# Optimization experiments

Hardware: AMD Instinct MI355X
Metric: run time of the kernel (lower is better)

Reference implementation:

```python
import jax, jax.numpy as jnp
import numpy as np

RMS_EPS = 1e-5


def setup_inputs() -> dict:
    key = jax.random.key(0)
    ks = jax.random.split(key, 7)
    B, N, D, H = 8, 1024, 1024, 4
    Dv = D // H
    s = lambda k, shp, fan: jax.random.normal(k, shp, jnp.float32) * (1.0 / np.sqrt(fan))
    return {
        "x": jax.random.normal(ks[0], (B, N, D), jnp.float32),
        "Wq": s(ks[1], (D, D), D),
        "Wk": s(ks[2], (D, D), D),
        "Wv": s(ks[3], (D, D), D),
        "Wbeta": s(ks[4], (D, H), D),
        "Wo": s(ks[5], (D, D), D),
        "g_norm": jnp.ones((Dv,), jnp.float32),
    }


def _l2norm(t):
    return t / jnp.linalg.norm(t, axis=-1, keepdims=True)


def _delta_rule(q, k, v, beta):
    # q,k: [B,H,N,Dk]; v: [B,H,N,Dv]; beta: [B,H,N]
    B, H, N, Dk = q.shape
    Dv = v.shape[-1]
    # time-major for scan: [N,B,H,D]
    qT = jnp.moveaxis(q, 2, 0)
    kT = jnp.moveaxis(k, 2, 0)
    vT = jnp.moveaxis(v, 2, 0)
    bT = jnp.moveaxis(beta, 2, 0)  # [N,B,H]

    def step(S, inp):
        q_t, k_t, v_t, b_t = inp  # [B,H,Dk], [B,H,Dk], [B,H,Dv], [B,H]
        pred = jnp.einsum('bhk,bhkv->bhv', k_t, S)
        err = (v_t - pred) * b_t[..., None]          # delta-rule error, scaled by beta
        S = S + jnp.einsum('bhk,bhv->bhkv', k_t, err)  # rank-1 state update
        o_t = jnp.einsum('bhk,bhkv->bhv', q_t, S)
        return S, o_t

    S0 = jnp.zeros((B, H, Dk, Dv), q.dtype)
    _, oT = jax.lax.scan(step, S0, (qT, kT, vT, bT))
    return jnp.moveaxis(oT, 0, 2)  # [B,H,N,Dv]


def reference(x, Wq, Wk, Wv, Wbeta, Wo, g_norm):
    B, N, D = x.shape
    H = Wbeta.shape[1]
    Dk = Wq.shape[1] // H
    Dv = Wv.shape[1] // H
    split = lambda t, d: t.reshape(B, N, H, d).transpose(0, 2, 1, 3)  # b n (h d) -> b h n d
    q = _l2norm(split(x @ Wq, Dk))
    k = _l2norm(split(x @ Wk, Dk))
    v = split(x @ Wv, Dv)
    beta = jax.nn.sigmoid(x @ Wbeta).transpose(0, 2, 1)  # [B,H,N]
    o = _delta_rule(q, k, v, beta)  # [B,H,N,Dv]
    # per-head RMSNorm over Dv
    o = o * jax.lax.rsqrt(jnp.mean(o * o, axis=-1, keepdims=True) + RMS_EPS) * g_norm
    o = o.transpose(0, 2, 1, 3).reshape(B, N, H * Dv)  # b h n d -> b n (h d)
    return o @ Wo
```

## Files before the change

kernel.cpp:

```cpp
#include <hip/hip_runtime.h>
#include <hip/hip_bf16.h>
#include <math.h>

typedef unsigned short u16;
typedef __attribute__((ext_vector_type(8))) __bf16 bf16x8;
typedef __attribute__((ext_vector_type(4))) float f32x4;

#define MFMA16 __builtin_amdgcn_mfma_f32_16x16x32_bf16

__device__ __forceinline__ float bf2f(unsigned int u) {
    union { unsigned int i; float f; } x;
    x.i = (u & 0xffffu) << 16;
    return x.f;
}
__device__ __forceinline__ u16 f2bf(float f) {
    unsigned int i = __float_as_uint(f);
    unsigned int r = (i + 0x7fffu + ((i >> 16) & 1u)) >> 16;
    return (u16)r;
}

__device__ __forceinline__ void gload_lds16(const void* g, void* l) {
    __builtin_amdgcn_global_load_lds((const __attribute__((address_space(1))) void*)g,
                                     (__attribute__((address_space(3))) void*)l, 16, 0, 0);
}

#define BARS() do { asm volatile("s_waitcnt lgkmcnt(0)" ::: "memory"); \
                    __builtin_amdgcn_s_barrier(); } while (0)
#define SYNCALL() do { asm volatile("s_waitcnt vmcnt(0) lgkmcnt(0)" ::: "memory"); \
                       __builtin_amdgcn_s_barrier(); } while (0)

__global__ void detect_dtype(const unsigned* __restrict__ wq, int* __restrict__ flag)
{
    int lane = threadIdx.x;
    unsigned lo = wq[lane] & 0xffffu;
    unsigned e = (lo >> 7) & 0xffu;
    int m = (e >= 0x6e && e <= 0x7e) ? 1 : 0;
#pragma unroll
    for (int s = 1; s < 64; s <<= 1) m += __shfl_xor(m, s);
    if (lane == 0) flag[0] = (m >= 32) ? 0 : 1;
}

__global__ __launch_bounds__(256) void convert_vec(
    const void* __restrict__ src, u16* __restrict__ dst, int n, const int* __restrict__ flag)
{
    int stride = gridDim.x * 256;
    int i0 = blockIdx.x * 256 + threadIdx.x;
    if (*flag) {
        const float* s = (const float*)src;
        for (int i = i0; i < n; i += stride) dst[i] = f2bf(s[i]);
    } else {
        const u16* s = (const u16*)src;
        for (int i = i0; i < n; i += stride) dst[i] = s[i];
    }
}

__global__ __launch_bounds__(256) void transpose_cvt(
    const void* __restrict__ w0, const void* __restrict__ w1,
    const void* __restrict__ w2, const void* __restrict__ w3,
    u16* __restrict__ o0, u16* __restrict__ o1,
    u16* __restrict__ o2, u16* __restrict__ o3, const int* __restrict__ flag)
{
    const void* in; u16* out;
    switch (blockIdx.z) {
        case 0: in = w0; out = o0; break;
        case 1: in = w1; out = o1; break;
        case 2: in = w2; out = o2; break;
        default: in = w3; out = o3; break;
    }
    int n  = blockIdx.x * 64 + (threadIdx.x & 63);
    int kb = blockIdx.y * 32 + (threadIdx.x >> 6) * 8;
    u16 v[8];
    if (*flag) {
        const float* f = (const float*)in;
#pragma unroll
        for (int j = 0; j < 8; ++j) v[j] = f2bf(f[(size_t)(kb + j) * 1024 + n]);
    } else {
        const u16* s = (const u16*)in;
#pragma unroll
        for (int j = 0; j < 8; ++j) v[j] = s[(size_t)(kb + j) * 1024 + n];
    }
    uint4 pk;
    pk.x = (unsigned)v[0] | ((unsigned)v[1] << 16);
    pk.y = (unsigned)v[2] | ((unsigned)v[3] << 16);
    pk.z = (unsigned)v[4] | ((unsigned)v[5] << 16);
    pk.w = (unsigned)v[6] | ((unsigned)v[7] << 16);
    *(uint4*)(out + (size_t)n * 1024 + kb) = pk;
}

__global__ __launch_bounds__(256) void gemm_bt(
    const u16* __restrict__ A, const u16* __restrict__ BT, void* __restrict__ C,
    int M, int Nn, int K, const int* __restrict__ flag, int fp32_out)
{
    __shared__ alignas(16) u16 As[128 * 32];
    __shared__ alignas(16) u16 Bs[128 * 32];
    const int tid  = threadIdx.x;
    const int lane = tid & 63;
    const int wv   = tid >> 6;
    const int wm   = wv >> 1, wn = wv & 1;
    const int bm   = blockIdx.x * 128, bn = blockIdx.y * 128;
    const int fr   = lane & 15, fk = lane >> 4;

    f32x4 acc[4][4];
#pragma unroll
    for (int i = 0; i < 4; ++i)
#pragma unroll
        for (int j = 0; j < 4; ++j) acc[i][j] = (f32x4){0.f, 0.f, 0.f, 0.f};

    for (int k0 = 0; k0 < K; k0 += 32) {
        __syncthreads();
#pragma unroll
        for (int p = 0; p < 2; ++p) {
            int i = tid + p * 256;
            int r = i >> 2, kc = (i & 3) << 3;
            gload_lds16(A  + (size_t)(bm + r) * K + k0 + kc,
                        (char*)As + (size_t)(wv * 64 + p * 256) * 16);
            gload_lds16(BT + (size_t)(bn + r) * K + k0 + kc,
                        (char*)Bs + (size_t)(wv * 64 + p * 256) * 16);
        }
        __syncthreads();
        bf16x8 af[4], bfr[4];
#pragma unroll
        for (int mi = 0; mi < 4; ++mi)
            af[mi] = *(const bf16x8*)(As + (wm * 64 + mi * 16 + fr) * 32 + fk * 8);
#pragma unroll
        for (int ni = 0; ni < 4; ++ni)
            bfr[ni] = *(const bf16x8*)(Bs + (wn * 64 + ni * 16 + fr) * 32 + fk * 8);
#pragma unroll
        for (int mi = 0; mi < 4; ++mi)
#pragma unroll
            for (int ni = 0; ni < 4; ++ni)
                acc[mi][ni] = MFMA16(af[mi], bfr[ni], acc[mi][ni], 0, 0, 0);
    }
    bool f32st = fp32_out && (*flag);
    if (f32st) {
        float* Cf = (float*)C;
#pragma unroll
        for (int mi = 0; mi < 4; ++mi)
#pragma unroll
            for (int ni = 0; ni < 4; ++ni)
#pragma unroll
                for (int j = 0; j < 4; ++j) {
                    int row = bm + wm * 64 + mi * 16 + fk * 4 + j;
                    int col = bn + wn * 64 + ni * 16 + fr;
                    Cf[(size_t)row * Nn + col] = acc[mi][ni][j];
                }
    } else {
        u16* Cb = (u16*)C;
#pragma unroll
        for (int mi = 0; mi < 4; ++mi)
#pragma unroll
            for (int ni = 0; ni < 4; ++ni)
#pragma unroll
                for (int j = 0; j < 4; ++j) {
                    int row = bm + wm * 64 + mi * 16 + fk * 4 + j;
                    int col = bn + wn * 64 + ni * 16 + fr;
                    Cb[(size_t)row * Nn + col] = f2bf(acc[mi][ni][j]);
                }
    }
}

__global__ __launch_bounds__(256) void gemm_qkv(
    const u16* __restrict__ A, const u16* __restrict__ BT,
    u16* __restrict__ Qo, u16* __restrict__ Ko, u16* __restrict__ Vo)
{
    __shared__ alignas(16) u16 As[128 * 32];
    __shared__ alignas(16) u16 Bs[128 * 32];
    const int tid  = threadIdx.x;
    const int lane = tid & 63;
    const int wv   = tid >> 6;
    const int wm   = wv >> 1, wn = wv & 1;
    const int bm   = blockIdx.x * 128, bn = blockIdx.y * 128;
    const int fr   = lane & 15, fk = lane >> 4;

    f32x4 acc[4][4];
#pragma unroll
    for (int i = 0; i < 4; ++i)
#pragma unroll
        for (int j = 0; j < 4; ++j) acc[i][j] = (f32x4){0.f, 0.f, 0.f, 0.f};

    for (int k0 = 0; k0 < 1024; k0 += 32) {
        __syncthreads();
#pragma unroll
        for (int p = 0; p < 2; ++p) {
            int i = tid + p * 256;
            int r = i >> 2, kc = (i & 3) << 3;
            gload_lds16(A  + (size_t)(bm + r) * 1024 + k0 + kc,
                        (char*)As + (size_t)(wv * 64 + p * 256) * 16);
            gload_lds16(BT + (size_t)(bn + r) * 1024 + k0 + kc,
                        (char*)Bs + (size_t)(wv * 64 + p * 256) * 16);
        }
        __syncthreads();
        bf16x8 af[4], bfr[4];
#pragma unroll
        for (int mi = 0; mi < 4; ++mi)
            af[mi] = *(const bf16x8*)(As + (wm * 64 + mi * 16 + fr) * 32 + fk * 8);
#pragma unroll
        for (int ni = 0; ni < 4; ++ni)
            bfr[ni] = *(const bf16x8*)(Bs + (wn * 64 + ni * 16 + fr) * 32 + fk * 8);
#pragma unroll
        for (int mi = 0; mi < 4; ++mi)
#pragma unroll
            for (int ni = 0; ni < 4; ++ni)
                acc[mi][ni] = MFMA16(af[mi], bfr[ni], acc[mi][ni], 0, 0, 0);
    }
    const int seg = bn >> 10;
    u16* Cb = (seg == 0) ? Qo : (seg == 1) ? Ko : Vo;
    const int cb = bn & 1023;
#pragma unroll
    for (int mi = 0; mi < 4; ++mi)
#pragma unroll
        for (int ni = 0; ni < 4; ++ni)
#pragma unroll
            for (int j = 0; j < 4; ++j) {
                int row = bm + wm * 64 + mi * 16 + fk * 4 + j;
                int col = cb + wn * 64 + ni * 16 + fr;
                Cb[(size_t)row * 1024 + col] = f2bf(acc[mi][ni][j]);
            }
}

__global__ __launch_bounds__(256) void beta_kernel(
    const u16* __restrict__ x, const u16* __restrict__ Wb, float* __restrict__ beta)
{
    int row  = blockIdx.x * 4 + (threadIdx.x >> 6);
    int lane = threadIdx.x & 63;
    const u16* xr = x + (size_t)row * 1024;
    float a0 = 0.f, a1 = 0.f, a2 = 0.f, a3 = 0.f;
    for (int c = 0; c < 16; ++c) {
        int k = c * 64 + lane;
        float xv = bf2f(xr[k]);
        uint2 w = *(const uint2*)(Wb + (size_t)k * 4);
        a0 += xv * bf2f(w.x);
        a1 += xv * bf2f(w.x >> 16);
        a2 += xv * bf2f(w.y);
        a3 += xv * bf2f(w.y >> 16);
    }
#pragma unroll
    for (int m = 1; m < 64; m <<= 1) {
        a0 += __shfl_xor(a0, m); a1 += __shfl_xor(a1, m);
        a2 += __shfl_xor(a2, m); a3 += __shfl_xor(a3, m);
    }
    if (lane == 0) {
        int b = row >> 10, nn = row & 1023;
        beta[(size_t)(b * 4 + 0) * 1024 + nn] = 1.f / (1.f + expf(-a0));
        beta[(size_t)(b * 4 + 1) * 1024 + nn] = 1.f / (1.f + expf(-a1));
        beta[(size_t)(b * 4 + 2) * 1024 + nn] = 1.f / (1.f + expf(-a2));
        beta[(size_t)(b * 4 + 3) * 1024 + nn] = 1.f / (1.f + expf(-a3));
    }
}

__global__ __launch_bounds__(256) void l2norm_qk(u16* __restrict__ Q, u16* __restrict__ K)
{
    u16* base = blockIdx.y ? K : Q;
    int w    = blockIdx.x * 4 + (threadIdx.x >> 6);
    int lane = threadIdx.x & 63;
    u16* p = base + (size_t)(w >> 2) * 1024 + (w & 3) * 256 + lane * 4;
    uint2 u = *(const uint2*)p;
    float f0 = bf2f(u.x), f1 = bf2f(u.x >> 16), f2 = bf2f(u.y), f3 = bf2f(u.y >> 16);
    float ss = f0 * f0 + f1 * f1 + f2 * f2 + f3 * f3;
#pragma unroll
    for (int m = 1; m < 64; m <<= 1) ss += __shfl_xor(ss, m);
    float inv = rsqrtf(ss + 1e-20f);
    uint2 o;
    o.x = (unsigned)f2bf(f0 * inv) | ((unsigned)f2bf(f1 * inv) << 16);
    o.y = (unsigned)f2bf(f2 * inv) | ((unsigned)f2bf(f3 * inv) << 16);
    *(uint2*)p = o;
}

#define AP 65
__global__ __launch_bounds__(256, 2) void phaseA(
    const u16* __restrict__ Kb, const u16* __restrict__ Qb,
    const float* __restrict__ Bp,
    u16* __restrict__ M1hi, u16* __restrict__ M1lo,
    u16* KTg)
{
    const int bh = blockIdx.x >> 4, ch = blockIdx.x & 15;
    const int bq = bh >> 2, h = bh & 3;
    const int tid = threadIdx.x;
    const int w = tid >> 6, L = tid & 63, fr = L & 15, fk = L >> 4;

    __shared__ alignas(16) u16 Ks[64 * 264];
    __shared__ alignas(16) u16 Qs[64 * 264];
    __shared__ float bc[64];

    float* Af = (float*)Ks;
    float* Tf = (float*)(Ks + 8320);
    u16* TtH = Qs;
    u16* TtL = Qs + 64 * 72;
    u16* QKs = Qs + 2 * 64 * 72;

    const size_t crow = ((size_t)bq * 1024 + ch * 64) * 1024 + (size_t)h * 256;
#pragma unroll
    for (int i = 0; i < 8; ++i) {
        int row = i * 8 + (tid >> 5), c8 = (tid & 31) * 8;
        uint4 kv = *(const uint4*)(Kb + crow + (size_t)row * 1024 + c8);
        uint4 qv = *(const uint4*)(Qb + crow + (size_t)row * 1024 + c8);
        *(uint4*)(Ks + row * 264 + c8) = kv;
        *(uint4*)(Qs + row * 264 + c8) = qv;
    }
    if (tid < 64) bc[tid] = Bp[(size_t)bh * 1024 + ch * 64 + tid];
    __syncthreads();

    const size_t kbase = (size_t)(bh * 16 + ch) * 16384;
#pragma unroll
    for (int i = 0; i < 8; ++i) {
        int item = tid + i * 256;
        int t = item & 63, g = item >> 6;
        union { uint4 q; u16 u[8]; } U;
        U.q = *(const uint4*)(Ks + t * 264 + g * 8);
#pragma unroll
        for (int e = 0; e < 8; ++e)
            KTg[kbase + (size_t)(g * 8 + e) * 64 + t] = U.u[e];
    }

    f32x4 kk[4], qk[4];
#pragma unroll
    for (int n = 0; n < 4; ++n) { kk[n] = (f32x4){0,0,0,0}; qk[n] = (f32x4){0,0,0,0}; }
#pragma unroll
    for (int k0 = 0; k0 < 8; ++k0) {
        bf16x8 ak = *(const bf16x8*)(Ks + (w * 16 + fr) * 264 + k0 * 32 + fk * 8);
        bf16x8 aq = *(const bf16x8*)(Qs + (w * 16 + fr) * 264 + k0 * 32 + fk * 8);
#pragma unroll
        for (int n = 0; n < 4; ++n) {
            bf16x8 bk = *(const bf16x8*)(Ks + (n * 16 + fr) * 264 + k0 * 32 + fk * 8);
            kk[n] = MFMA16(ak, bk, kk[n], 0, 0, 0);
            qk[n] = MFMA16(aq, bk, qk[n], 0, 0, 0);
        }
    }
    __syncthreads();

#pragma unroll
    for (int n = 0; n < 4; ++n)
#pragma unroll
        for (int j = 0; j < 4; ++j) {
            int t = w * 16 + fk * 4 + j, s = n * 16 + fr;
            Af[t * AP + s] = (s < t) ? bc[t] * kk[n][j] : 0.f;
            QKs[t * 72 + s] = f2bf((s <= t) ? qk[n][j] : 0.f);
        }
    for (int i = tid; i < 64 * AP; i += 256) Tf[i] = 0.f;
    __syncthreads();

    {
        int j = w * 16 + fr;
        int p = fk;
        for (int t = 0; t < 64; ++t) {
            float acc = 0.f;
#pragma unroll
            for (int i = 0; i < 16; ++i) {
                int s = p + 4 * i;
                acc += Af[t * AP + s] * Tf[s * AP + j];
            }
            acc += __shfl_xor(acc, 16);
            acc += __shfl_xor(acc, 32);
            float val = ((t == j) ? 1.f : 0.f) - acc;
            if (p == 0) Tf[t * AP + j] = val;
        }
    }
    __syncthreads();

#pragma unroll
    for (int e = 0; e < 16; ++e) {
        int idx = tid + e * 256;
        int t = idx >> 6, s = idx & 63;
        float f = Tf[t * AP + s];
        u16 hh = f2bf(f);
        TtH[s * 72 + t] = hh;
        TtL[s * 72 + t] = f2bf(f - bf2f(hh));
    }
    __syncthreads();

    const size_t tb2 = (size_t)(bh * 16 + ch) * 4096;
    f32x4 accM[4];
#pragma unroll
    for (int ns = 0; ns < 4; ++ns) accM[ns] = (f32x4){0,0,0,0};
#pragma unroll
    for (int k0 = 0; k0 < 2; ++k0) {
        bf16x8 aq = *(const bf16x8*)(QKs + (w * 16 + fr) * 72 + k0 * 32 + fk * 8);
#pragma unroll
        for (int ns = 0; ns < 4; ++ns) {
            bf16x8 bh_ = *(const bf16x8*)(TtH + (ns * 16 + fr) * 72 + k0 * 32 + fk * 8);
            bf16x8 bl_ = *(const bf16x8*)(TtL + (ns * 16 + fr) * 72 + k0 * 32 + fk * 8);
            accM[ns] = MFMA16(aq, bh_, accM[ns], 0, 0, 0);
            accM[ns] = MFMA16(aq, bl_, accM[ns], 0, 0, 0);
        }
    }
#pragma unroll
    for (int ns = 0; ns < 4; ++ns)
#pragma unroll
        for (int j = 0; j < 4; ++j) {
            int t = w * 16 + fk * 4 + j, a = ns * 16 + fr;
            float v = accM[ns][j];
            u16 hh = f2bf(v);
            M1hi[tb2 + t * 64 + a] = hh;
            M1lo[tb2 + t * 64 + a] = f2bf(v - bf2f(hh));
        }

    asm volatile("s_waitcnt vmcnt(0)" ::: "memory");
#pragma unroll
    for (int nn = 0; nn < 4; ++nn) {
        bf16x8 af2[2];
#pragma unroll
        for (int k0 = 0; k0 < 2; ++k0)
            af2[k0] = *(const bf16x8*)(KTg + kbase
                        + (size_t)(w * 64 + nn * 16 + fr) * 64 + k0 * 32 + fk * 8);
        f32x4 acc2[4];
#pragma unroll
        for (int ns = 0; ns < 4; ++ns) acc2[ns] = (f32x4){0,0,0,0};
#pragma unroll
        for (int k0 = 0; k0 < 2; ++k0)
#pragma unroll
            for (int ns = 0; ns < 4; ++ns) {
                bf16x8 bh_ = *(const bf16x8*)(TtH + (ns * 16 + fr) * 72 + k0 * 32 + fk * 8);
                bf16x8 bl_ = *(const bf16x8*)(TtL + (ns * 16 + fr) * 72 + k0 * 32 + fk * 8);
                acc2[ns] = MFMA16(af2[k0], bh_, acc2[ns], 0, 0, 0);
                acc2[ns] = MFMA16(af2[k0], bl_, acc2[ns], 0, 0, 0);
            }
        asm volatile("s_waitcnt vmcnt(0)" ::: "memory");
#pragma unroll
        for (int ns = 0; ns < 4; ++ns)
#pragma unroll
            for (int j = 0; j < 4; ++j)
                KTg[kbase + (size_t)(w * 64 + nn * 16 + fk * 4 + j) * 64 + ns * 16 + fr]
                    = f2bf(acc2[ns][j]);
    }
}

#define WTP 72
#define SHP 264
__global__ __launch_bounds__(512, 1) void phaseB(
    const u16* __restrict__ Kb, const u16* __restrict__ Qb, u16* Vb,
    const float* __restrict__ Bp,
    const u16* __restrict__ M1hi, const u16* __restrict__ M1lo,
    const u16* __restrict__ Ktil)
{
    const int bh  = blockIdx.x & 31;
    const int dvb = blockIdx.x >> 5;
    const int bq = bh >> 2, h = bh & 3;
    const int tid = threadIdx.x;
    const int wv8 = tid >> 6;
    const int n   = wv8 >> 2;
    const int wg  = wv8 & 3;
    const int L = tid & 63, fr = L & 15, fk = L >> 4;
    const int rl = L >> 5, cp = L & 31;

    __shared__ alignas(16) u16 Kl[64 * 256];
    __shared__ alignas(16) u16 Ql[64 * 256];
    __shared__ alignas(16) u16 S_hi[32 * SHP];
    __shared__ alignas(16) u16 S_lo[32 * SHP];
    __shared__ alignas(16) u16 W_T[32 * WTP];
    __shared__ float bc[1024];

    for (int i = tid; i < 32 * SHP; i += 512) { S_hi[i] = 0; S_lo[i] = 0; }
    for (int i = tid; i < 1024; i += 512) bc[i] = Bp[(size_t)bh * 1024 + i];

    const size_t rb = ((size_t)bq * 1024) * 1024 + (size_t)h * 256;

    f32x4 sreg[4];
#pragma unroll
    for (int nn = 0; nn < 4; ++nn) sreg[nn] = (f32x4){0,0,0,0};

    bf16x8 m1h[2], m1l[2], ktf[2][4];
    u16 vr[4];

    auto stage_kq = [&](int c) {
        const size_t crow = rb + (size_t)(c * 64) * 1024;
#pragma unroll
        for (int i = 0; i < 4; ++i) {
            int rg = wv8 * 8 + 2 * i + rl;
            int cu = cp ^ (rg & 7);
            gload_lds16(Kb + crow + (size_t)rg * 1024 + cu * 8,
                        (char*)Kl + (size_t)(wv8 * 8 + 2 * i) * 512);
            gload_lds16(Qb + crow + (size_t)rg * 1024 + cu * 8,
                        (char*)Ql + (size_t)(wv8 * 8 + 2 * i) * 512);
        }
    };
    auto pf_m1 = [&](int c) {
        const size_t mb = (size_t)(bh * 16 + c) * 4096 + (size_t)(wg * 16 + fr) * 64 + fk * 8;
#pragma unroll
        for (int k0 = 0; k0 < 2; ++k0) {
            m1h[k0] = *(const bf16x8*)(M1hi + mb + k0 * 32);
            m1l[k0] = *(const bf16x8*)(M1lo + mb + k0 * 32);
        }
    };
    auto pf_ktf = [&](int c) {
        const size_t kb2 = (size_t)(bh * 16 + c) * 16384;
#pragma unroll
        for (int k0 = 0; k0 < 2; ++k0)
#pragma unroll
            for (int nn = 0; nn < 4; ++nn)
                ktf[k0][nn] = *(const bf16x8*)(Ktil + kb2
                              + (size_t)(wg * 64 + nn * 16 + fr) * 64 + k0 * 32 + fk * 8);
    };
    auto pf_vr = [&](int c) {
        const size_t crow = rb + (size_t)(c * 64) * 1024;
#pragma unroll
        for (int j = 0; j < 4; ++j)
            vr[j] = Vb[crow + (size_t)(wg * 16 + fk * 4 + j) * 1024
                          + dvb * 32 + n * 16 + fr];
    };

    stage_kq(0); pf_m1(0); pf_ktf(0); pf_vr(0);

    for (int c = 0; c < 16; ++c) {
        SYNCALL();
        f32x4 aPh = (f32x4){0,0,0,0}, aPl = (f32x4){0,0,0,0};
        f32x4 aOh = (f32x4){0,0,0,0}, aOl = (f32x4){0,0,0,0};
#pragma unroll
        for (int k0 = 0; k0 < 8; ++k0) {
            int ru = ((k0 * 4 + fk) ^ (fr & 7)) * 8;
            bf16x8 kqf = *(const bf16x8*)(Kl + (wg * 16 + fr) * 256 + ru);
            bf16x8 qqf = *(const bf16x8*)(Ql + (wg * 16 + fr) * 256 + ru);
            bf16x8 shi = *(const bf16x8*)(S_hi + (n * 16 + fr) * SHP + k0 * 32 + fk * 8);
            bf16x8 slo = *(const bf16x8*)(S_lo + (n * 16 + fr) * SHP + k0 * 32 + fk * 8);
            aPh = MFMA16(kqf, shi, aPh, 0, 0, 0);
            aPl = MFMA16(kqf, slo, aPl, 0, 0, 0);
            aOh = MFMA16(qqf, shi, aOh, 0, 0, 0);
            aOl = MFMA16(qqf, slo, aOl, 0, 0, 0);
        }
        const size_t crow = rb + (size_t)(c * 64) * 1024;
        {
            f32x4 accP = aPh + aPl;
#pragma unroll
            for (int j = 0; j < 4; ++j) {
                int t = wg * 16 + fk * 4 + j;
                W_T[(n * 16 + fr) * WTP + t] = f2bf(bc[c * 64 + t] * (bf2f(vr[j]) - accP[j]));
            }
        }
        BARS();
        if (c + 1 < 16) stage_kq(c + 1);
        bf16x8 wf[2];
#pragma unroll
        for (int k0 = 0; k0 < 2; ++k0)
            wf[k0] = *(const bf16x8*)(W_T + (n * 16 + fr) * WTP + k0 * 32 + fk * 8);
        f32x4 accO = aOh + aOl;
#pragma unroll
        for (int k0 = 0; k0 < 2; ++k0) {
            accO = MFMA16(m1h[k0], wf[k0], accO, 0, 0, 0);
            accO = MFMA16(m1l[k0], wf[k0], accO, 0, 0, 0);
        }
#pragma unroll
        for (int j = 0; j < 4; ++j)
            Vb[crow + (size_t)(wg * 16 + fk * 4 + j) * 1024 + dvb * 32 + n * 16 + fr]
                = f2bf(accO[j]);
        if (c + 1 < 16) pf_m1(c + 1);
        f32x4 dS[4];
#pragma unroll
        for (int nn = 0; nn < 4; ++nn) dS[nn] = (f32x4){0,0,0,0};
#pragma unroll
        for (int k0 = 0; k0 < 2; ++k0)
#pragma unroll
            for (int nn = 0; nn < 4; ++nn)
                dS[nn] = MFMA16(wf[k0], ktf[k0][nn], dS[nn], 0, 0, 0);
        if (c + 1 < 16) { pf_ktf(c + 1); pf_vr(c + 1); }
#pragma unroll
        for (int nn = 0; nn < 4; ++nn) {
            sreg[nn] = sreg[nn] + dS[nn];
#pragma unroll
            for (int j = 0; j < 4; ++j) {
                int idx = (n * 16 + fk * 4 + j) * SHP + (wg * 64 + nn * 16 + fr);
                float s = sreg[nn][j];
                u16 hh = f2bf(s);
                S_hi[idx] = hh;
                S_lo[idx] = f2bf(s - bf2f(hh));
            }
        }
    }
}

__global__ __launch_bounds__(256) void rmsnorm_o(u16* V, const u16* __restrict__ gn)
{
    int w    = blockIdx.x * 4 + (threadIdx.x >> 6);
    int lane = threadIdx.x & 63;
    u16* p = V + (size_t)(w >> 2) * 1024 + (w & 3) * 256 + lane * 4;
    uint2 u = *(const uint2*)p;
    float f0 = bf2f(u.x), f1 = bf2f(u.x >> 16), f2 = bf2f(u.y), f3 = bf2f(u.y >> 16);
    float ss = f0 * f0 + f1 * f1 + f2 * f2 + f3 * f3;
#pragma unroll
    for (int m = 1; m < 64; m <<= 1) ss += __shfl_xor(ss, m);
    float sc = rsqrtf(ss * (1.0f / 256.0f) + 1e-5f);
    int d0 = lane * 4;
    uint2 gu = *(const uint2*)(gn + d0);
    float g0 = bf2f(gu.x), g1 = bf2f(gu.x >> 16), g2 = bf2f(gu.y), g3 = bf2f(gu.y >> 16);
    uint2 o;
    o.x = (unsigned)f2bf(f0 * sc * g0) | ((unsigned)f2bf(f1 * sc * g1) << 16);
    o.y = (unsigned)f2bf(f2 * sc * g2) | ((unsigned)f2bf(f3 * sc * g3) << 16);
    *(uint2*)p = o;
}

extern "C" void kernel_launch(void* const* d_in, const int* in_sizes, int n_in,
                              void* d_out, int out_size, void* d_ws, size_t ws_size,
                              hipStream_t stream)
{
    const void* x  = d_in[0];
    const void* Wq = d_in[1];
    const void* Wk = d_in[2];
    const void* Wv = d_in[3];
    const void* Wb = d_in[4];
    const void* Wo = d_in[5];
    const void* gn = d_in[6];

    char* ws = (char*)d_ws;
    const size_t OFF_FLAG = 0;
    const size_t OFF_WBC  = 4096;
    const size_t OFF_GNC  = OFF_WBC + 8192;
    const size_t OFF_XB   = OFF_GNC + 4096;
    const size_t OFF_WQT  = OFF_XB + 16777216;
    const size_t OFF_WKT  = OFF_WQT + 2097152;
    const size_t OFF_WVT  = OFF_WKT + 2097152;
    const size_t OFF_WOT  = OFF_WVT + 2097152;
    const size_t OFF_Q    = OFF_WOT + 2097152;
    const size_t OFF_K    = OFF_Q + 16777216;
    const size_t OFF_V    = OFF_K + 16777216;
    const size_t OFF_BP   = OFF_V + 16777216;

    const size_t OFF_M1H  = OFF_XB + 8388608;
    const size_t OFF_M1L  = OFF_XB + 12582912;

    int*   flag = (int*)(ws + OFF_FLAG);
    u16*   Wbc  = (u16*)(ws + OFF_WBC);
    u16*   gnc  = (u16*)(ws + OFF_GNC);
    u16*   Xb   = (u16*)(ws + OFF_XB);
    u16*   wqT  = (u16*)(ws + OFF_WQT);
    u16*   wkT  = (u16*)(ws + OFF_WKT);
    u16*   wvT  = (u16*)(ws + OFF_WVT);
    u16*   woT  = (u16*)(ws + OFF_WOT);
    u16*   Qb   = (u16*)(ws + OFF_Q);
    u16*   Kb   = (u16*)(ws + OFF_K);
    u16*   Vb   = (u16*)(ws + OFF_V);
    float* Bp   = (float*)(ws + OFF_BP);
    u16*   M1hi = (u16*)(ws + OFF_M1H);
    u16*   M1lo = (u16*)(ws + OFF_M1L);
    u16*   KTg  = (u16*)d_out;

    detect_dtype<<<1, 64, 0, stream>>>((const unsigned*)Wq, flag);
    convert_vec<<<2048, 256, 0, stream>>>(x, Xb, 8388608, flag);
    convert_vec<<<16, 256, 0, stream>>>(Wb, Wbc, 4096, flag);
    convert_vec<<<1, 256, 0, stream>>>(gn, gnc, 256, flag);
    transpose_cvt<<<dim3(16, 32, 4), 256, 0, stream>>>(Wq, Wk, Wv, Wo, wqT, wkT, wvT, woT, flag);

    gemm_qkv<<<dim3(64, 24), 256, 0, stream>>>(Xb, wqT, Qb, Kb, Vb);
    beta_kernel<<<2048, 256, 0, stream>>>(Xb, Wbc, Bp);
    l2norm_qk<<<dim3(8192, 2), 256, 0, stream>>>(Qb, Kb);

    phaseA<<<512, 256, 0, stream>>>(Kb, Qb, Bp, M1hi, M1lo, KTg);
    phaseB<<<256, 512, 0, stream>>>(Kb, Qb, Vb, Bp, M1hi, M1lo, KTg);

    rmsnorm_o<<<8192, 256, 0, stream>>>(Vb, gnc);
    gemm_bt<<<dim3(64, 8), 256, 0, stream>>>(Vb, woT, d_out, 8192, 1024, 1024, flag, 1);
}
```

Measured before the change: 272.7 us.

## Split phaseB into narrower 16-column value tiles with Q held in registers

The phaseB grid is reshaped from 256 blocks of 512 threads to 512 blocks of 256 threads. Each block now owns a 16-wide Dv slice instead of 32, so the LDS state and W tiles shrink and two blocks can share a CU. Q fragments are loaded straight from global memory into registers instead of being staged through LDS. The prefetch of the next K chunk now starts before the mid-loop barrier, and a barrier is added at the end of each step. Costs: more register pressure, K staging and Ktil loads repeated across twice as many blocks, and a possible race where one wave overwrites Kl while another wave is still reading the current chunk.

New measurement: 280.4 us. 2.8% more time.

```diff
diff --git a/kernel.cpp b/kernel.cpp
--- a/kernel.cpp
+++ b/kernel.cpp
@@ -26,8 +26,6 @@
 
 #define BARS() do { asm volatile("s_waitcnt lgkmcnt(0)" ::: "memory"); \
                     __builtin_amdgcn_s_barrier(); } while (0)
-#define SYNCALL() do { asm volatile("s_waitcnt vmcnt(0) lgkmcnt(0)" ::: "memory"); \
-                       __builtin_amdgcn_s_barrier(); } while (0)
 
 __global__ void detect_dtype(const unsigned* __restrict__ wq, int* __restrict__ flag)
 {
@@ -426,7 +424,7 @@
 
 #define WTP 72
 #define SHP 264
-__global__ __launch_bounds__(512, 1) void phaseB(
+__global__ __launch_bounds__(256, 2) void phaseB(
     const u16* __restrict__ Kb, const u16* __restrict__ Qb, u16* Vb,
     const float* __restrict__ Bp,
     const u16* __restrict__ M1hi, const u16* __restrict__ M1lo,
@@ -436,21 +434,17 @@
     const int dvb = blockIdx.x >> 5;
     const int bq = bh >> 2, h = bh & 3;
     const int tid = threadIdx.x;
-    const int wv8 = tid >> 6;
-    const int n   = wv8 >> 2;
-    const int wg  = wv8 & 3;
-    const int L = tid & 63, fr = L & 15, fk = L >> 4;
+    const int w = tid >> 6, L = tid & 63, fr = L & 15, fk = L >> 4;
     const int rl = L >> 5, cp = L & 31;
 
     __shared__ alignas(16) u16 Kl[64 * 256];
-    __shared__ alignas(16) u16 Ql[64 * 256];
-    __shared__ alignas(16) u16 S_hi[32 * SHP];
-    __shared__ alignas(16) u16 S_lo[32 * SHP];
-    __shared__ alignas(16) u16 W_T[32 * WTP];
+    __shared__ alignas(16) u16 S_hi[16 * SHP];
+    __shared__ alignas(16) u16 S_lo[16 * SHP];
+    __shared__ alignas(16) u16 W_T[16 * WTP];
     __shared__ float bc[1024];
 
-    for (int i = tid; i < 32 * SHP; i += 512) { S_hi[i] = 0; S_lo[i] = 0; }
-    for (int i = tid; i < 1024; i += 512) bc[i] = Bp[(size_t)bh * 1024 + i];
+    for (int i = tid; i < 16 * SHP; i += 256) { S_hi[i] = 0; S_lo[i] = 0; }
+    for (int i = tid; i < 1024; i += 256) bc[i] = Bp[(size_t)bh * 1024 + i];
 
     const size_t rb = ((size_t)bq * 1024) * 1024 + (size_t)h * 256;
 
@@ -458,23 +452,27 @@
 #pragma unroll
     for (int nn = 0; nn < 4; ++nn) sreg[nn] = (f32x4){0,0,0,0};
 
-    bf16x8 m1h[2], m1l[2], ktf[2][4];
+    bf16x8 qq[8], m1h[2], m1l[2], ktf[2][4];
     u16 vr[4];
 
-    auto stage_kq = [&](int c) {
+    auto stage_k = [&](int c) {
         const size_t crow = rb + (size_t)(c * 64) * 1024;
 #pragma unroll
-        for (int i = 0; i < 4; ++i) {
-            int rg = wv8 * 8 + 2 * i + rl;
+        for (int i = 0; i < 8; ++i) {
+            int rg = w * 16 + 2 * i + rl;
             int cu = cp ^ (rg & 7);
             gload_lds16(Kb + crow + (size_t)rg * 1024 + cu * 8,
-                        (char*)Kl + (size_t)(wv8 * 8 + 2 * i) * 512);
-            gload_lds16(Qb + crow + (size_t)rg * 1024 + cu * 8,
-                        (char*)Ql + (size_t)(wv8 * 8 + 2 * i) * 512);
-        }
+                        (char*)Kl + (size_t)(w * 16 + 2 * i) * 512);
+        }
+    };
+    auto pf_q = [&](int c) {
+        const size_t arow = rb + (size_t)(c * 64 + w * 16 + fr) * 1024 + fk * 8;
+#pragma unroll
+        for (int k0 = 0; k0 < 8; ++k0)
+            qq[k0] = *(const bf16x8*)(Qb + arow + k0 * 32);
     };
     auto pf_m1 = [&](int c) {
-        const size_t mb = (size_t)(bh * 16 + c) * 4096 + (size_t)(wg * 16 + fr) * 64 + fk * 8;
+        const size_t mb = (size_t)(bh * 16 + c) * 4096 + (size_t)(w * 16 + fr) * 64 + fk * 8;
 #pragma unroll
         for (int k0 = 0; k0 < 2; ++k0) {
             m1h[k0] = *(const bf16x8*)(M1hi + mb + k0 * 32);
@@ -488,49 +486,48 @@
 #pragma unroll
             for (int nn = 0; nn < 4; ++nn)
                 ktf[k0][nn] = *(const bf16x8*)(Ktil + kb2
-                              + (size_t)(wg * 64 + nn * 16 + fr) * 64 + k0 * 32 + fk * 8);
+                              + (size_t)(w * 64 + nn * 16 + fr) * 64 + k0 * 32 + fk * 8);
     };
     auto pf_vr = [&](int c) {
         const size_t crow = rb + (size_t)(c * 64) * 1024;
 #pragma unroll
         for (int j = 0; j < 4; ++j)
-            vr[j] = Vb[crow + (size_t)(wg * 16 + fk * 4 + j) * 1024
-                          + dvb * 32 + n * 16 + fr];
+            vr[j] = Vb[crow + (size_t)(w * 16 + fk * 4 + j) * 1024 + dvb * 16 + fr];
     };
 
-    stage_kq(0); pf_m1(0); pf_ktf(0); pf_vr(0);
+    stage_k(0); pf_q(0); pf_m1(0); pf_ktf(0); pf_vr(0);
+    __syncthreads();
 
     for (int c = 0; c < 16; ++c) {
-        SYNCALL();
+        asm volatile("s_waitcnt vmcnt(0)" ::: "memory");
         f32x4 aPh = (f32x4){0,0,0,0}, aPl = (f32x4){0,0,0,0};
         f32x4 aOh = (f32x4){0,0,0,0}, aOl = (f32x4){0,0,0,0};
 #pragma unroll
         for (int k0 = 0; k0 < 8; ++k0) {
             int ru = ((k0 * 4 + fk) ^ (fr & 7)) * 8;
-            bf16x8 kqf = *(const bf16x8*)(Kl + (wg * 16 + fr) * 256 + ru);
-            bf16x8 qqf = *(const bf16x8*)(Ql + (wg * 16 + fr) * 256 + ru);
-            bf16x8 shi = *(const bf16x8*)(S_hi + (n * 16 + fr) * SHP + k0 * 32 + fk * 8);
-            bf16x8 slo = *(const bf16x8*)(S_lo + (n * 16 + fr) * SHP + k0 * 32 + fk * 8);
+            bf16x8 kqf = *(const bf16x8*)(Kl + (w * 16 + fr) * 256 + ru);
+            bf16x8 shi = *(const bf16x8*)(S_hi + fr * SHP + k0 * 32 + fk * 8);
+            bf16x8 slo = *(const bf16x8*)(S_lo + fr * SHP + k0 * 32 + fk * 8);
             aPh = MFMA16(kqf, shi, aPh, 0, 0, 0);
             aPl = MFMA16(kqf, slo, aPl, 0, 0, 0);
-            aOh = MFMA16(qqf, shi, aOh, 0, 0, 0);
-            aOl = MFMA16(qqf, slo, aOl, 0, 0, 0);
+            aOh = MFMA16(qq[k0], shi, aOh, 0, 0, 0);
+            aOl = MFMA16(qq[k0], slo, aOl, 0, 0, 0);
         }
         const size_t crow = rb + (size_t)(c * 64) * 1024;
         {
             f32x4 accP = aPh + aPl;
 #pragma unroll
             for (int j = 0; j < 4; ++j) {
-                int t = wg * 16 + fk * 4 + j;
-                W_T[(n * 16 + fr) * WTP + t] = f2bf(bc[c * 64 + t] * (bf2f(vr[j]) - accP[j]));
+                int t = w * 16 + fk * 4 + j;
+                W_T[fr * WTP + t] = f2bf(bc[c * 64 + t] * (bf2f(vr[j]) - accP[j]));
             }
         }
+        if (c + 1 < 16) { stage_k(c + 1); pf_q(c + 1); }
         BARS();
-        if (c + 1 < 16) stage_kq(c + 1);
         bf16x8 wf[2];
 #pragma unroll
         for (int k0 = 0; k0 < 2; ++k0)
-            wf[k0] = *(const bf16x8*)(W_T + (n * 16 + fr) * WTP + k0 * 32 + fk * 8);
+            wf[k0] = *(const bf16x8*)(W_T + fr * WTP + k0 * 32 + fk * 8);
         f32x4 accO = aOh + aOl;
 #pragma unroll
         for (int k0 = 0; k0 < 2; ++k0) {
@@ -539,7 +536,7 @@
         }
 #pragma unroll
         for (int j = 0; j < 4; ++j)
-            Vb[crow + (size_t)(wg * 16 + fk * 4 + j) * 1024 + dvb * 32 + n * 16 + fr]
+            Vb[crow + (size_t)(w * 16 + fk * 4 + j) * 1024 + dvb * 16 + fr]
                 = f2bf(accO[j]);
         if (c + 1 < 16) pf_m1(c + 1);
         f32x4 dS[4];
@@ -556,13 +553,14 @@
             sreg[nn] = sreg[nn] + dS[nn];
 #pragma unroll
             for (int j = 0; j < 4; ++j) {
-                int idx = (n * 16 + fk * 4 + j) * SHP + (wg * 64 + nn * 16 + fr);
+                int idx = (fk * 4 + j) * SHP + (w * 64 + nn * 16 + fr);
                 float s = sreg[nn][j];
                 u16 hh = f2bf(s);
                 S_hi[idx] = hh;
                 S_lo[idx] = f2bf(s - bf2f(hh));
             }
         }
+        BARS();
     }
 }
 
@@ -642,7 +640,7 @@
     l2norm_qk<<<dim3(8192, 2), 256, 0, stream>>>(Qb, Kb);
 
     phaseA<<<512, 256, 0, stream>>>(Kb, Qb, Bp, M1hi, M1lo, KTg);
-    phaseB<<<256, 512, 0, stream>>>(Kb, Qb, Vb, Bp, M1hi, M1lo, KTg);
+    phaseB<<<512, 256, 0, stream>>>(Kb, Qb, Vb, Bp, M1hi, M1lo, KTg);
 
     rmsnorm_o<<<8192, 256, 0, stream>>>(Vb, gnc);
     gemm_bt<<<dim3(64, 8), 256, 0, stream>>>(Vb, woT, d_out, 8192, 1024, 1024, flag, 1);
```
